# Kernel optimization log

Hardware: AMD Instinct MI355X
Metric: run time of the kernel (lower is better)

## Reference

```python
import jax, jax.numpy as jnp
import numpy as np

N_NODES = 100000
N_EDGES = 3200000
NEG_SLOPE = 0.2  # PyG GATConv default


def setup_inputs() -> dict:
    key = jax.random.key(0)
    ks = jax.random.split(key, 10)
    x = jax.random.normal(ks[0], (N_NODES, 2), dtype=jnp.float32)
    src = jax.random.randint(ks[1], (N_EDGES,), 0, N_NODES)
    dst = jax.random.randint(ks[2], (N_EDGES,), 0, N_NODES)
    edge_index = jnp.stack([src, dst]).astype(jnp.int64)
    edge_attr = jax.random.normal(ks[3], (N_EDGES, 4), dtype=jnp.float32)
    # layer 1: in=2, heads=4, out_per_head=8
    W1 = jax.random.normal(ks[4], (2, 32), dtype=jnp.float32) * 0.5
    att_src1 = jax.random.normal(ks[5], (4, 8), dtype=jnp.float32) * 0.3
    att_dst1 = jax.random.normal(ks[6], (4, 8), dtype=jnp.float32) * 0.3
    b1 = jnp.zeros((32,), dtype=jnp.float32)
    # layer 2: in=32, heads=1, out_per_head=2
    W2 = jax.random.normal(ks[7], (32, 2), dtype=jnp.float32) * 0.2
    att_src2 = jax.random.normal(ks[8], (1, 2), dtype=jnp.float32) * 0.3
    att_dst2 = jax.random.normal(ks[9], (1, 2), dtype=jnp.float32) * 0.3
    b2 = jnp.zeros((2,), dtype=jnp.float32)
    return {"x": x, "edge_index": edge_index, "edge_attr": edge_attr,
            "W1": W1, "att_src1": att_src1, "att_dst1": att_dst1, "b1": b1,
            "W2": W2, "att_src2": att_src2, "att_dst2": att_dst2, "b2": b2}


def _gat_conv(x, W, att_src, att_dst, bias, src, dst, heads, out_ch, concat, n):
    h = (x @ W).reshape(n, heads, out_ch)            # [N,H,C]
    a_s = (h * att_src).sum(-1)                       # [N,H]
    a_d = (h * att_dst).sum(-1)                       # [N,H]
    e = jax.nn.leaky_relu(a_s[src] + a_d[dst], NEG_SLOPE)  # [E,H]
    m = jax.ops.segment_max(e, dst, num_segments=n)   # stable softmax over dst groups
    ee = jnp.exp(e - m[dst])
    s = jax.ops.segment_sum(ee, dst, num_segments=n)
    alpha = ee / (s[dst] + 1e-16)                     # [E,H]
    out = jax.ops.segment_sum(h[src] * alpha[:, :, None], dst, num_segments=n)  # [N,H,C]
    out = out.reshape(n, heads * out_ch) if concat else out.mean(axis=1)
    return out + bias, alpha


def reference(x, edge_index, edge_attr, W1, att_src1, att_dst1, b1,
              W2, att_src2, att_dst2, b2):
    # edge_attr is accepted but ignored: GATConv was built without edge_dim.
    n = x.shape[0]
    loop = jnp.arange(n, dtype=edge_index.dtype)      # add_self_loops=True (PyG default)
    src = jnp.concatenate([edge_index[0], loop])
    dst = jnp.concatenate([edge_index[1], loop])
    h, alpha1 = _gat_conv(x, W1, att_src1, att_dst1, b1, src, dst, 4, 8, True, n)
    h = jax.nn.elu(h)
    out, alpha2 = _gat_conv(h, W2, att_src2, att_dst2, b2, src, dst, 1, 2, False, n)
    return out, alpha1, alpha2
```

## Files before the change

### kernel.cpp

```cpp
#include <hip/hip_runtime.h>
#include <hip/hip_fp16.h>
#include <math.h>

#define NEG_SLOPE 0.2f
#define BW 512
#define BSH 9
#define CAP 18432
#define NB_MAX 256

typedef float f4v __attribute__((ext_vector_type(4)));
typedef float f2v __attribute__((ext_vector_type(2)));
typedef int   i2v __attribute__((ext_vector_type(2)));

__device__ __forceinline__ float lrelu(float v) {
    return v > 0.0f ? v : NEG_SLOPE * v;
}
__device__ __forceinline__ float pack2h(float a, float b) {
    __half2 h = __floats2half2_rn(a, b);
    return *reinterpret_cast<float*>(&h);
}
__device__ __forceinline__ float2 unpack2h(float f) {
    __half2 h = *reinterpret_cast<__half2*>(&f);
    return __half22float2(h);
}
__device__ __forceinline__ void nt_store4(float4 v, float4* p) {
    f4v x = {v.x, v.y, v.z, v.w};
    __builtin_nontemporal_store(x, (f4v*)p);
}
__device__ __forceinline__ void nt_store2(float2 v, float2* p) {
    f2v x = {v.x, v.y};
    __builtin_nontemporal_store(x, (f2v*)p);
}

__global__ __launch_bounds__(256) void k_l1_node(
    const float* __restrict__ x, const float* __restrict__ W1,
    const float* __restrict__ asw, const float* __restrict__ adw,
    float4* __restrict__ ga, float4* __restrict__ spack,
    float2* __restrict__ dpack2, int* __restrict__ bucketCursor,
    int nb, int n)
{
    int i = blockIdx.x * blockDim.x + threadIdx.x;
    if (i < nb) bucketCursor[i] = 0;
    if (i >= n) return;
    float2 xv = ((const float2*)x)[i];
    float as[4] = {0.f, 0.f, 0.f, 0.f};
    float ad[4] = {0.f, 0.f, 0.f, 0.f};
    #pragma unroll
    for (int j = 0; j < 32; ++j) {
        float h = xv.x * W1[j] + xv.y * W1[32 + j];
        as[j >> 3] += h * asw[j];
        ad[j >> 3] += h * adw[j];
    }
    float p01 = pack2h(as[0], as[1]), p23 = pack2h(as[2], as[3]);
    ga[i] = make_float4(p01, p23, xv.x, xv.y);
    spack[i] = make_float4(p01, p23, 0.f, 0.f);
    dpack2[2 * i] = make_float2(pack2h(ad[0], ad[1]), pack2h(ad[2], ad[3]));
}

__global__ __launch_bounds__(256) void k_binA(
    const int* __restrict__ ei, int* __restrict__ bucketCursor,
    unsigned int* __restrict__ binned, int E, int Et, int nb)
{
    __shared__ int cnt[NB_MAX], lscan[NB_MAX], base[NB_MAX], lcur[NB_MAX];
    __shared__ unsigned int staging[4096];
    __shared__ short sbk[4096];
    int t = threadIdx.x;
    int c0 = blockIdx.x * 4096;
    unsigned int ent[16];
    short bb[16];
    #pragma unroll
    for (int k = 0; k < 16; ++k) {
        int e = c0 + k * 256 + t;
        int s, d;
        if (e < E) {
            s = __builtin_nontemporal_load(&ei[e]);
            d = __builtin_nontemporal_load(&ei[E + e]);
        } else { s = e - E; d = s; }
        bool valid = e < Et;
        bb[k] = valid ? (short)(d >> BSH) : (short)(-1);
        ent[k] = ((unsigned int)s << BSH) | (unsigned int)(d & (BW - 1));
    }
    cnt[t] = 0;
    __syncthreads();
    #pragma unroll
    for (int k = 0; k < 16; ++k)
        if (bb[k] >= 0) atomicAdd(&cnt[bb[k]], 1);
    __syncthreads();
    int c = cnt[t];
    lscan[t] = c;
    __syncthreads();
    for (int off = 1; off < 256; off <<= 1) {
        int v = (t >= off) ? lscan[t - off] : 0;
        __syncthreads();
        lscan[t] += v;
        __syncthreads();
    }
    int tot = lscan[255];
    int ex = lscan[t] - c;
    __syncthreads();
    lscan[t] = ex;
    lcur[t] = ex;
    if (t < nb && c > 0) base[t] = atomicAdd(&bucketCursor[t], c);
    __syncthreads();
    #pragma unroll
    for (int k = 0; k < 16; ++k)
        if (bb[k] >= 0) {
            int p = atomicAdd(&lcur[bb[k]], 1);
            staging[p] = ent[k];
            sbk[p] = bb[k];
        }
    __syncthreads();
    for (int j = t; j < tot; j += 256) {
        int lo = sbk[j];
        __builtin_nontemporal_store(staging[j],
            &binned[(size_t)lo * CAP + base[lo] + (j - lscan[lo])]);
    }
}

__global__ __launch_bounds__(1024) void k_binB(
    const unsigned int* __restrict__ binned, const int* __restrict__ bucketCursor,
    int* __restrict__ sorted, int2* __restrict__ rowrange, int n, int nb)
{
    __shared__ int cnt[BW], cur[BW];
    int t = threadIdx.x;
    int b = blockIdx.x;
    int m = bucketCursor[b];
    size_t base = (size_t)b * CAP;
    int node0 = b << BSH;
    if (t < BW) cnt[t] = 0;
    __syncthreads();
    for (int i = t; i < m; i += 1024)
        atomicAdd(&cnt[binned[base + i] & (BW - 1)], 1);
    __syncthreads();
    int deg = (t < BW) ? cnt[t] : 0;
    for (int off = 1; off < BW; off <<= 1) {
        int v = (t >= off && t < BW) ? cnt[t - off] : 0;
        __syncthreads();
        if (t < BW) cnt[t] += v;
        __syncthreads();
    }
    if (t < BW) {
        int ex = cnt[t] - deg;
        cur[t] = ex;
        int node = node0 + t;
        if (node < n)
            rowrange[node] = make_int2((int)base + ex, (int)base + ex + deg);
    }
    __syncthreads();
    for (int i = t; i < m; i += 1024) {
        unsigned int en = binned[base + i];
        int dl = (int)(en & (BW - 1));
        int p = atomicAdd(&cur[dl], 1);
        sorted[base + p] = (int)(en >> BSH);
    }
}

__global__ __launch_bounds__(256) void k_l1_gather(
    const int2* __restrict__ rowrange, const int* __restrict__ sorted,
    const float4* __restrict__ ga, float2* __restrict__ dpack2,
    const float* __restrict__ W1, const float* __restrict__ b1,
    const float* __restrict__ W2,
    const float* __restrict__ asw2, const float* __restrict__ adw2,
    float4* __restrict__ pk2f, float4* __restrict__ spack,
    __half* __restrict__ dpk2h, int n)
{
    int t = blockIdx.x * blockDim.x + threadIdx.x;
    int d = t >> 3, q = t & 7;
    if (d >= n) return;
    int2 rr = rowrange[d];
    int beg = rr.x, end = rr.y;
    float2 adp = dpack2[2 * d];
    float2 ad01 = unpack2h(adp.x), ad23 = unpack2h(adp.y);
    float see[4] = {0.f, 0.f, 0.f, 0.f};
    float sx0[4] = {0.f, 0.f, 0.f, 0.f};
    float sx1[4] = {0.f, 0.f, 0.f, 0.f};
    int i = beg + q;
    for (; i + 8 < end; i += 16) {
        int s0 = sorted[i], s1 = sorted[i + 8];
        float4 v0 = ga[s0], v1 = ga[s1];
        #pragma unroll
        for (int k = 0; k < 2; ++k) {
            float4 v = k ? v1 : v0;
            float2 a01 = unpack2h(v.x), a23 = unpack2h(v.y);
            float e0 = __expf(lrelu(a01.x + ad01.x));
            float e1 = __expf(lrelu(a01.y + ad01.y));
            float e2 = __expf(lrelu(a23.x + ad23.x));
            float e3 = __expf(lrelu(a23.y + ad23.y));
            see[0] += e0; sx0[0] += e0 * v.z; sx1[0] += e0 * v.w;
            see[1] += e1; sx0[1] += e1 * v.z; sx1[1] += e1 * v.w;
            see[2] += e2; sx0[2] += e2 * v.z; sx1[2] += e2 * v.w;
            see[3] += e3; sx0[3] += e3 * v.z; sx1[3] += e3 * v.w;
        }
    }
    for (; i < end; i += 8) {
        float4 v = ga[sorted[i]];
        float2 a01 = unpack2h(v.x), a23 = unpack2h(v.y);
        float e0 = __expf(lrelu(a01.x + ad01.x));
        float e1 = __expf(lrelu(a01.y + ad01.y));
        float e2 = __expf(lrelu(a23.x + ad23.x));
        float e3 = __expf(lrelu(a23.y + ad23.y));
        see[0] += e0; sx0[0] += e0 * v.z; sx1[0] += e0 * v.w;
        see[1] += e1; sx0[1] += e1 * v.z; sx1[1] += e1 * v.w;
        see[2] += e2; sx0[2] += e2 * v.z; sx1[2] += e2 * v.w;
        see[3] += e3; sx0[3] += e3 * v.z; sx1[3] += e3 * v.w;
    }
    #pragma unroll
    for (int h = 0; h < 4; ++h) {
        see[h] += __shfl_xor(see[h], 1);
        sx0[h] += __shfl_xor(sx0[h], 1);
        sx1[h] += __shfl_xor(sx1[h], 1);
        see[h] += __shfl_xor(see[h], 2);
        sx0[h] += __shfl_xor(sx0[h], 2);
        sx1[h] += __shfl_xor(sx1[h], 2);
        see[h] += __shfl_xor(see[h], 4);
        sx0[h] += __shfl_xor(sx0[h], 4);
        sx1[h] += __shfl_xor(sx1[h], 4);
    }
    if (q) return;
    float rs[4];
    #pragma unroll
    for (int h = 0; h < 4; ++h) rs[h] = 1.0f / (see[h] + 1e-16f);
    dpack2[2 * d + 1] = make_float2(pack2h(rs[0], rs[1]), pack2h(rs[2], rs[3]));
    float h20 = 0.f, h21 = 0.f;
    #pragma unroll
    for (int j = 0; j < 32; ++j) {
        int h = j >> 3;
        float num = W1[j] * sx0[h] + W1[32 + j] * sx1[h];
        float o = num * rs[h] + b1[j];
        float he = o > 0.f ? o : expm1f(o);
        h20 += he * W2[2 * j];
        h21 += he * W2[2 * j + 1];
    }
    float as2 = h20 * asw2[0] + h21 * asw2[1];
    float ad2 = h20 * adw2[0] + h21 * adw2[1];
    pk2f[d] = make_float4(as2, h20, h21, ad2);
    ((float*)&spack[d])[2] = as2;
    dpk2h[2 * d] = __float2half(ad2);
}

__global__ __launch_bounds__(256) void k_l2_gather(
    const int2* __restrict__ rowrange, const int* __restrict__ sorted,
    const float4* __restrict__ pk2f, const float* __restrict__ b2,
    __half* __restrict__ dpk2h, float* __restrict__ out, int n)
{
    int t = blockIdx.x * blockDim.x + threadIdx.x;
    int d = t >> 3, q = t & 7;
    if (d >= n) return;
    int2 rr = rowrange[d];
    int beg = rr.x, end = rr.y;
    float ad2 = pk2f[d].w;
    float se = 0.f, a0 = 0.f, a1 = 0.f;
    int i = beg + q;
    for (; i + 8 < end; i += 16) {
        int s0 = sorted[i], s1 = sorted[i + 8];
        float4 p0 = pk2f[s0], p1 = pk2f[s1];
        float e0 = __expf(lrelu(p0.x + ad2));
        float e1 = __expf(lrelu(p1.x + ad2));
        se += e0 + e1;
        a0 += e0 * p0.y + e1 * p1.y;
        a1 += e0 * p0.z + e1 * p1.z;
    }
    for (; i < end; i += 8) {
        float4 p = pk2f[sorted[i]];
        float ee = __expf(lrelu(p.x + ad2));
        se += ee; a0 += ee * p.y; a1 += ee * p.z;
    }
    se += __shfl_xor(se, 1); a0 += __shfl_xor(a0, 1); a1 += __shfl_xor(a1, 1);
    se += __shfl_xor(se, 2); a0 += __shfl_xor(a0, 2); a1 += __shfl_xor(a1, 2);
    se += __shfl_xor(se, 4); a0 += __shfl_xor(a0, 4); a1 += __shfl_xor(a1, 4);
    if (q) return;
    float rs2 = 1.0f / (se + 1e-16f);
    dpk2h[2 * d + 1] = __float2half(rs2);
    ((float2*)out)[d] = make_float2(a0 * rs2 + b2[0], a1 * rs2 + b2[1]);
}

__global__ __launch_bounds__(256) void k_alpha(
    const int* __restrict__ ei, const float4* __restrict__ spack,
    const float4* __restrict__ dpack, const float* __restrict__ dpk2hf,
    float4* __restrict__ alpha1, float2* __restrict__ alpha2_2, int E, int Et)
{
    __shared__ float4 lds[512];
    int t = threadIdx.x;
    int base = blockIdx.x * 512;
    int e0 = base + 2 * t;
    if (e0 < Et) {
        int s0, d0, s1, d1;
        if (e0 < E) {
            i2v ss = __builtin_nontemporal_load((const i2v*)(ei + e0));
            i2v dd = __builtin_nontemporal_load((const i2v*)(ei + E + e0));
            s0 = ss.x; s1 = ss.y; d0 = dd.x; d1 = dd.y;
        } else {
            s0 = e0 - E; d0 = s0; s1 = s0 + 1; d1 = s1;
        }
        float4 sp0 = spack[s0], sp1 = spack[s1];
        float4 dp0 = dpack[d0], dp1 = dpack[d1];
        float  dh0 = dpk2hf[d0], dh1 = dpk2hf[d1];

        float2 a01, a23, b01, b23, r01, r23, ar;
        float4 al;
        a01 = unpack2h(sp0.x); a23 = unpack2h(sp0.y);
        b01 = unpack2h(dp0.x); b23 = unpack2h(dp0.y);
        r01 = unpack2h(dp0.z); r23 = unpack2h(dp0.w);
        al.x = __expf(lrelu(a01.x + b01.x)) * r01.x;
        al.y = __expf(lrelu(a01.y + b01.y)) * r01.y;
        al.z = __expf(lrelu(a23.x + b23.x)) * r23.x;
        al.w = __expf(lrelu(a23.y + b23.y)) * r23.y;
        lds[t] = al;
        ar = unpack2h(dh0);
        float o20 = __expf(lrelu(sp0.z + ar.x)) * ar.y;
        a01 = unpack2h(sp1.x); a23 = unpack2h(sp1.y);
        b01 = unpack2h(dp1.x); b23 = unpack2h(dp1.y);
        r01 = unpack2h(dp1.z); r23 = unpack2h(dp1.w);
        al.x = __expf(lrelu(a01.x + b01.x)) * r01.x;
        al.y = __expf(lrelu(a01.y + b01.y)) * r01.y;
        al.z = __expf(lrelu(a23.x + b23.x)) * r23.x;
        al.w = __expf(lrelu(a23.y + b23.y)) * r23.y;
        lds[256 + t] = al;
        ar = unpack2h(dh1);
        float o21 = __expf(lrelu(sp1.z + ar.x)) * ar.y;
        nt_store2(make_float2(o20, o21), &alpha2_2[(base >> 1) + t]);
    }
    __syncthreads();
    int v0 = t;
    if (base + v0 < Et)
        nt_store4(lds[(v0 & 1) * 256 + (v0 >> 1)], &alpha1[base + v0]);
    int v1 = t + 256;
    if (base + v1 < Et)
        nt_store4(lds[(v1 & 1) * 256 + (v1 >> 1)], &alpha1[base + v1]);
}

extern "C" void kernel_launch(void* const* d_in, const int* in_sizes, int n_in,
                              void* d_out, int out_size, void* d_ws, size_t ws_size,
                              hipStream_t stream)
{
    const float* x   = (const float*)d_in[0];
    const int*   ei  = (const int*)d_in[1];
    const float* W1  = (const float*)d_in[3];
    const float* as1 = (const float*)d_in[4];
    const float* ad1 = (const float*)d_in[5];
    const float* b1  = (const float*)d_in[6];
    const float* W2  = (const float*)d_in[7];
    const float* as2 = (const float*)d_in[8];
    const float* ad2 = (const float*)d_in[9];
    const float* b2  = (const float*)d_in[10];

    const int n  = in_sizes[0] / 2;
    const int E  = in_sizes[1] / 2;
    const int Et = E + n;
    const int nb = (n + BW - 1) >> BSH;

    char* w = (char*)d_ws;
    float4* ga    = (float4*)w;  w += (size_t)n * sizeof(float4);
    float4* spack = (float4*)w;  w += (size_t)n * sizeof(float4);
    float4* dpack = (float4*)w;  w += (size_t)n * sizeof(float4);
    float4* pk2f  = (float4*)w;  w += (size_t)n * sizeof(float4);
    float*  dpk2hf= (float*)w;   w += (size_t)n * sizeof(float);
    int2*   rowrange = (int2*)w; w += (size_t)n * sizeof(int2);
    int*    sorted   = (int*)w;  w += (size_t)nb * CAP * sizeof(int);
    int*    bucketCursor = (int*)w; w += (size_t)nb * sizeof(int);

    float*  out    = (float*)d_out;
    float4* alpha1 = (float4*)(out + (size_t)n * 2);
    float2* alpha2_2 = (float2*)(alpha1 + (size_t)Et);
    unsigned int* binned = (unsigned int*)alpha1;

    dim3 blk(256);
    int gn   = (n + 255) / 256;
    int gn8  = (8 * n + 255) / 256;
    int gA   = (Et + 4095) / 4096;
    int gAl  = (Et + 511) / 512;

    k_l1_node  <<<gn,  blk, 0, stream>>>(x, W1, as1, ad1, ga, spack,
                                         (float2*)dpack, bucketCursor, nb, n);
    k_binA     <<<gA,  blk, 0, stream>>>(ei, bucketCursor, binned, E, Et, nb);
    k_binB     <<<nb, dim3(1024), 0, stream>>>(binned, bucketCursor, sorted, rowrange, n, nb);
    k_l1_gather<<<gn8, blk, 0, stream>>>(rowrange, sorted, ga, (float2*)dpack,
                                         W1, b1, W2, as2, ad2, pk2f, spack,
                                         (__half*)dpk2hf, n);
    k_l2_gather<<<gn8, blk, 0, stream>>>(rowrange, sorted, pk2f, b2,
                                         (__half*)dpk2hf, out, n);
    k_alpha    <<<gAl, blk, 0, stream>>>(ei, spack, dpack, dpk2hf,
                                         alpha1, alpha2_2, E, Et);
}
```

Baseline: 284.3 us.

## Interleave per-node src/dst attention records and vectorize edge-index loads in binning

Three per-node side arrays (source attention, destination attention plus reciprocal sums, and half-precision layer-2 values) are merged into one interleaved 32-byte record per node. The alpha kernel's destination lookups then fall in adjacent memory within the same cache line, which should cut the random cache lines touched per edge. The binning kernel now loads edge indices two at a time as int2, halving load instruction count. The cost is a wider, more tightly coupled record layout that relies on specific half-word offsets and on E being even for alignment.

```diff
diff --git a/kernel.cpp b/kernel.cpp
--- a/kernel.cpp
+++ b/kernel.cpp
@@ -32,12 +32,12 @@
     __builtin_nontemporal_store(x, (f2v*)p);
 }
 
+
 __global__ __launch_bounds__(256) void k_l1_node(
     const float* __restrict__ x, const float* __restrict__ W1,
     const float* __restrict__ asw, const float* __restrict__ adw,
-    float4* __restrict__ ga, float4* __restrict__ spack,
-    float2* __restrict__ dpack2, int* __restrict__ bucketCursor,
-    int nb, int n)
+    float4* __restrict__ ga, float4* __restrict__ npk,
+    int* __restrict__ bucketCursor, int nb, int n)
 {
     int i = blockIdx.x * blockDim.x + threadIdx.x;
     if (i < nb) bucketCursor[i] = 0;
@@ -53,8 +53,8 @@
     }
     float p01 = pack2h(as[0], as[1]), p23 = pack2h(as[2], as[3]);
     ga[i] = make_float4(p01, p23, xv.x, xv.y);
-    spack[i] = make_float4(p01, p23, 0.f, 0.f);
-    dpack2[2 * i] = make_float2(pack2h(ad[0], ad[1]), pack2h(ad[2], ad[3]));
+    npk[2 * i]     = make_float4(p01, p23, 0.f, 0.f);
+    npk[2 * i + 1] = make_float4(pack2h(ad[0], ad[1]), pack2h(ad[2], ad[3]), 0.f, 0.f);
 }
 
 __global__ __launch_bounds__(256) void k_binA(
@@ -69,16 +69,19 @@
     unsigned int ent[16];
     short bb[16];
     #pragma unroll
-    for (int k = 0; k < 16; ++k) {
-        int e = c0 + k * 256 + t;
-        int s, d;
-        if (e < E) {
-            s = __builtin_nontemporal_load(&ei[e]);
-            d = __builtin_nontemporal_load(&ei[E + e]);
-        } else { s = e - E; d = s; }
-        bool valid = e < Et;
-        bb[k] = valid ? (short)(d >> BSH) : (short)(-1);
-        ent[k] = ((unsigned int)s << BSH) | (unsigned int)(d & (BW - 1));
+    for (int k = 0; k < 8; ++k) {
+        int e0 = c0 + 2 * (k * 256 + t);
+        int s0, d0, s1, d1;
+        if (e0 < E) {
+            i2v ss = __builtin_nontemporal_load((const i2v*)(ei + e0));
+            i2v dd = __builtin_nontemporal_load((const i2v*)(ei + E + e0));
+            s0 = ss.x; s1 = ss.y; d0 = dd.x; d1 = dd.y;
+        } else { s0 = e0 - E; d0 = s0; s1 = s0 + 1; d1 = s1; }
+        bool valid = e0 < Et;
+        bb[2 * k]     = valid ? (short)(d0 >> BSH) : (short)(-1);
+        bb[2 * k + 1] = valid ? (short)(d1 >> BSH) : (short)(-1);
+        ent[2 * k]     = ((unsigned int)s0 << BSH) | (unsigned int)(d0 & (BW - 1));
+        ent[2 * k + 1] = ((unsigned int)s1 << BSH) | (unsigned int)(d1 & (BW - 1));
     }
     cnt[t] = 0;
     __syncthreads();
@@ -157,19 +160,18 @@
 
 __global__ __launch_bounds__(256) void k_l1_gather(
     const int2* __restrict__ rowrange, const int* __restrict__ sorted,
-    const float4* __restrict__ ga, float2* __restrict__ dpack2,
+    const float4* __restrict__ ga, float4* __restrict__ npk,
     const float* __restrict__ W1, const float* __restrict__ b1,
     const float* __restrict__ W2,
     const float* __restrict__ asw2, const float* __restrict__ adw2,
-    float4* __restrict__ pk2f, float4* __restrict__ spack,
-    __half* __restrict__ dpk2h, int n)
+    float4* __restrict__ pk2f, int n)
 {
     int t = blockIdx.x * blockDim.x + threadIdx.x;
     int d = t >> 3, q = t & 7;
     if (d >= n) return;
     int2 rr = rowrange[d];
     int beg = rr.x, end = rr.y;
-    float2 adp = dpack2[2 * d];
+    float2 adp = *(const float2*)&npk[2 * d + 1];
     float2 ad01 = unpack2h(adp.x), ad23 = unpack2h(adp.y);
     float see[4] = {0.f, 0.f, 0.f, 0.f};
     float sx0[4] = {0.f, 0.f, 0.f, 0.f};
@@ -220,7 +222,7 @@
     float rs[4];
     #pragma unroll
     for (int h = 0; h < 4; ++h) rs[h] = 1.0f / (see[h] + 1e-16f);
-    dpack2[2 * d + 1] = make_float2(pack2h(rs[0], rs[1]), pack2h(rs[2], rs[3]));
+    ((float2*)&npk[2 * d + 1])[1] = make_float2(pack2h(rs[0], rs[1]), pack2h(rs[2], rs[3]));
     float h20 = 0.f, h21 = 0.f;
     #pragma unroll
     for (int j = 0; j < 32; ++j) {
@@ -234,14 +236,14 @@
     float as2 = h20 * asw2[0] + h21 * asw2[1];
     float ad2 = h20 * adw2[0] + h21 * adw2[1];
     pk2f[d] = make_float4(as2, h20, h21, ad2);
-    ((float*)&spack[d])[2] = as2;
-    dpk2h[2 * d] = __float2half(ad2);
+    ((float*)&npk[2 * d])[2] = as2;
+    ((__half*)&npk[2 * d])[6] = __float2half(ad2);
 }
 
 __global__ __launch_bounds__(256) void k_l2_gather(
     const int2* __restrict__ rowrange, const int* __restrict__ sorted,
     const float4* __restrict__ pk2f, const float* __restrict__ b2,
-    __half* __restrict__ dpk2h, float* __restrict__ out, int n)
+    float4* __restrict__ npk, float* __restrict__ out, int n)
 {
     int t = blockIdx.x * blockDim.x + threadIdx.x;
     int d = t >> 3, q = t & 7;
@@ -270,13 +272,12 @@
     se += __shfl_xor(se, 4); a0 += __shfl_xor(a0, 4); a1 += __shfl_xor(a1, 4);
     if (q) return;
     float rs2 = 1.0f / (se + 1e-16f);
-    dpk2h[2 * d + 1] = __float2half(rs2);
+    ((__half*)&npk[2 * d])[7] = __float2half(rs2);
     ((float2*)out)[d] = make_float2(a0 * rs2 + b2[0], a1 * rs2 + b2[1]);
 }
 
 __global__ __launch_bounds__(256) void k_alpha(
-    const int* __restrict__ ei, const float4* __restrict__ spack,
-    const float4* __restrict__ dpack, const float* __restrict__ dpk2hf,
+    const int* __restrict__ ei, const float4* __restrict__ npk,
     float4* __restrict__ alpha1, float2* __restrict__ alpha2_2, int E, int Et)
 {
     __shared__ float4 lds[512];
@@ -292,32 +293,33 @@
         } else {
             s0 = e0 - E; d0 = s0; s1 = s0 + 1; d1 = s1;
         }
-        float4 sp0 = spack[s0], sp1 = spack[s1];
-        float4 dp0 = dpack[d0], dp1 = dpack[d1];
-        float  dh0 = dpk2hf[d0], dh1 = dpk2hf[d1];
+        float4 lo0 = npk[2 * s0], lo1 = npk[2 * s1];
+        float4 hi0 = npk[2 * d0 + 1], hi1 = npk[2 * d1 + 1];
+        float  w30 = ((const float*)npk)[8 * d0 + 3];
+        float  w31 = ((const float*)npk)[8 * d1 + 3];
 
         float2 a01, a23, b01, b23, r01, r23, ar;
         float4 al;
-        a01 = unpack2h(sp0.x); a23 = unpack2h(sp0.y);
-        b01 = unpack2h(dp0.x); b23 = unpack2h(dp0.y);
-        r01 = unpack2h(dp0.z); r23 = unpack2h(dp0.w);
+        a01 = unpack2h(lo0.x); a23 = unpack2h(lo0.y);
+        b01 = unpack2h(hi0.x); b23 = unpack2h(hi0.y);
+        r01 = unpack2h(hi0.z); r23 = unpack2h(hi0.w);
         al.x = __expf(lrelu(a01.x + b01.x)) * r01.x;
         al.y = __expf(lrelu(a01.y + b01.y)) * r01.y;
         al.z = __expf(lrelu(a23.x + b23.x)) * r23.x;
         al.w = __expf(lrelu(a23.y + b23.y)) * r23.y;
         lds[t] = al;
-        ar = unpack2h(dh0);
-        float o20 = __expf(lrelu(sp0.z + ar.x)) * ar.y;
-        a01 = unpack2h(sp1.x); a23 = unpack2h(sp1.y);
-        b01 = unpack2h(dp1.x); b23 = unpack2h(dp1.y);
-        r01 = unpack2h(dp1.z); r23 = unpack2h(dp1.w);
+        ar = unpack2h(w30);
+        float o20 = __expf(lrelu(lo0.z + ar.x)) * ar.y;
+        a01 = unpack2h(lo1.x); a23 = unpack2h(lo1.y);
+        b01 = unpack2h(hi1.x); b23 = unpack2h(hi1.y);
+        r01 = unpack2h(hi1.z); r23 = unpack2h(hi1.w);
         al.x = __expf(lrelu(a01.x + b01.x)) * r01.x;
         al.y = __expf(lrelu(a01.y + b01.y)) * r01.y;
         al.z = __expf(lrelu(a23.x + b23.x)) * r23.x;
         al.w = __expf(lrelu(a23.y + b23.y)) * r23.y;
         lds[256 + t] = al;
-        ar = unpack2h(dh1);
-        float o21 = __expf(lrelu(sp1.z + ar.x)) * ar.y;
+        ar = unpack2h(w31);
+        float o21 = __expf(lrelu(lo1.z + ar.x)) * ar.y;
         nt_store2(make_float2(o20, o21), &alpha2_2[(base >> 1) + t]);
     }
     __syncthreads();
@@ -351,10 +353,8 @@
 
     char* w = (char*)d_ws;
     float4* ga    = (float4*)w;  w += (size_t)n * sizeof(float4);
-    float4* spack = (float4*)w;  w += (size_t)n * sizeof(float4);
-    float4* dpack = (float4*)w;  w += (size_t)n * sizeof(float4);
+    float4* npk   = (float4*)w;  w += (size_t)n * 2 * sizeof(float4);
     float4* pk2f  = (float4*)w;  w += (size_t)n * sizeof(float4);
-    float*  dpk2hf= (float*)w;   w += (size_t)n * sizeof(float);
     int2*   rowrange = (int2*)w; w += (size_t)n * sizeof(int2);
     int*    sorted   = (int*)w;  w += (size_t)nb * CAP * sizeof(int);
     int*    bucketCursor = (int*)w; w += (size_t)nb * sizeof(int);
@@ -370,15 +370,14 @@
     int gA   = (Et + 4095) / 4096;
     int gAl  = (Et + 511) / 512;
 
-    k_l1_node  <<<gn,  blk, 0, stream>>>(x, W1, as1, ad1, ga, spack,
-                                         (float2*)dpack, bucketCursor, nb, n);
+    k_l1_node  <<<gn,  blk, 0, stream>>>(x, W1, as1, ad1, ga, npk,
+                                         bucketCursor, nb, n);
     k_binA     <<<gA,  blk, 0, stream>>>(ei, bucketCursor, binned, E, Et, nb);
     k_binB     <<<nb, dim3(1024), 0, stream>>>(binned, bucketCursor, sorted, rowrange, n, nb);
-    k_l1_gather<<<gn8, blk, 0, stream>>>(rowrange, sorted, ga, (float2*)dpack,
-                                         W1, b1, W2, as2, ad2, pk2f, spack,
-                                         (__half*)dpk2hf, n);
+    k_l1_gather<<<gn8, blk, 0, stream>>>(rowrange, sorted, ga, npk,
+                                         W1, b1, W2, as2, ad2, pk2f, n);
     k_l2_gather<<<gn8, blk, 0, stream>>>(rowrange, sorted, pk2f, b2,
-                                         (__half*)dpk2hf, out, n);
-    k_alpha    <<<gAl, blk, 0, stream>>>(ei, spack, dpack, dpk2hf,
+                                         npk, out, n);
+    k_alpha    <<<gAl, blk, 0, stream>>>(ei, npk,
                                          alpha1, alpha2_2, E, Et);
 }
```

Measured after the change: 275.7 us. 1.03x faster.
